# Kernel tuning notes

Hardware: AMD Instinct MI355X
Metric: run time of the kernel (lower is better)

The kernel has to match this reference:

```python
import jax, jax.numpy as jnp
jax.config.update("jax_enable_x64", True)
import numpy as np

B, S, D, H = 2, 1024, 1024, 16
DEPTH = D // H  # 64


def setup_inputs() -> dict:
    key = jax.random.key(0)
    ks = jax.random.split(key, 12)
    inp = {
        "q": jax.random.normal(ks[0], (B, S, D), jnp.float32),
        "k": jax.random.normal(ks[1], (B, S, D), jnp.float32),
        "v": jax.random.normal(ks[2], (B, S - 1, D), jnp.float32),
        "e": jnp.zeros((1,), jnp.float32),  # unused by the layer
        "mask": jax.random.randint(ks[3], (B, S - 1, S - 1), 0, 2, jnp.int32),
        "Wq": jax.random.normal(ks[4], (D, D), jnp.float32) * 0.02,
        "bq": jnp.zeros((D,), jnp.float32),
        "Wk": jax.random.normal(ks[5], (D, D), jnp.float32) * 0.02,
        "bk": jnp.zeros((D,), jnp.float32),
        "Wv": jax.random.normal(ks[6], (D, D), jnp.float32) * 0.02,
        "bv": jnp.zeros((D,), jnp.float32),
        "Wo": jax.random.normal(ks[7], (D, D), jnp.float32) * 0.02,
        "bo": jnp.zeros((D,), jnp.float32),
    }
    return inp


def _split_heads(x, b):
    # [b, s, D] -> [b, H, s, DEPTH]
    return x.reshape(b, -1, H, DEPTH).transpose(0, 2, 1, 3)


def reference(q, k, v, e, mask, Wq, bq, Wk, bk, Wv, bv, Wo, bo):
    b = q.shape[0]
    qh = _split_heads(q @ Wq + bq, b)  # [b,H,S,dh]
    kh = _split_heads(k @ Wk + bk, b)  # [b,H,S,dh]
    vh = _split_heads(v @ Wv + bv, b)  # [b,H,S-1,dh]
    # QK^T then asymmetric offset slice [1:, :-1]
    scores = jnp.einsum("bhqd,bhkd->bhqk", qh, kh)[:, :, 1:, :-1]  # [b,H,S-1,S-1]
    inv_sqrt_dk = 1.0 / jnp.sqrt(jnp.float32(DEPTH))
    nl_qk = jax.nn.relu(scores * inv_sqrt_dk).astype(jnp.float64)
    nl_qk = nl_qk + mask[:, None, :, :].astype(jnp.float64) * (-1e9)
    att_weights = jax.nn.softmax(nl_qk, axis=-1)  # fp64, [b,H,S-1,S-1]
    out = jnp.einsum("bhqk,bhkd->bhqd", att_weights, vh.astype(jnp.float64))
    out = out.transpose(0, 2, 1, 3).reshape(b, -1, H * DEPTH)  # [b,S-1,D]
    output = out.astype(jnp.float32) @ Wo + bo
    return (output, att_weights)
```

## Files before the change

kernel.cpp:

```cpp
#include <hip/hip_runtime.h>
#include <math.h>

#define HN 16
#define SEQ 1024
#define DMODEL 1024
#define DH 64
#define SM1 1023

typedef float  f32x4  __attribute__((ext_vector_type(4)));
typedef __bf16 bf16x8 __attribute__((ext_vector_type(8)));

template<int MODE>
__global__ __launch_bounds__(256)
void gemm_mfma_kernel(const float* __restrict__ X, const float* __restrict__ W,
                      const float* __restrict__ bias, float* __restrict__ out32,
                      __bf16* __restrict__ outHi, __bf16* __restrict__ outLo,
                      int M, int rows)
{
    __shared__ __align__(16) __bf16 As[2][4096];
    __shared__ __align__(16) __bf16 Bs[2][4096];

    const int t  = threadIdx.x;
    const int w  = t >> 6, l = t & 63;
    const int lr = l & 15, ls = l >> 4;
    const int m0 = blockIdx.y * 64, n0 = blockIdx.x * 64;
    const int sr  = t >> 2;
    const int skq = t & 3;
    const bool arow_ok = (m0 + sr < M);

    f32x4 acc[4];
#pragma unroll
    for (int ct = 0; ct < 4; ++ct) acc[ct] = f32x4{0.f, 0.f, 0.f, 0.f};

    const int ar   = w * 16 + lr;
    const int a_hi = ar * 128 + (((2 * ls    ) ^ (ar & 7)) << 4);
    const int a_lo = ar * 128 + (((2 * ls + 1) ^ (ar & 7)) << 4);
    const int st_hi = sr * 128 + (((2 * skq    ) ^ (sr & 7)) << 4);
    const int st_lo = sr * 128 + (((2 * skq + 1) ^ (sr & 7)) << 4);

    float4 xv0, xv1;
    float  wv[8];

    auto LOADT = [&](int k0) {
        if (arow_ok) {
            xv0 = *(const float4*)&X[(size_t)(m0 + sr) * DMODEL + k0 + skq * 8];
            xv1 = *(const float4*)&X[(size_t)(m0 + sr) * DMODEL + k0 + skq * 8 + 4];
        } else {
            xv0 = float4{0.f, 0.f, 0.f, 0.f};
            xv1 = float4{0.f, 0.f, 0.f, 0.f};
        }
#pragma unroll
        for (int e = 0; e < 8; ++e)
            wv[e] = W[(size_t)(k0 + skq * 8 + e) * DMODEL + n0 + sr];
    };
    auto WRITET = [&](int buf) {
        float xa[8] = {xv0.x, xv0.y, xv0.z, xv0.w, xv1.x, xv1.y, xv1.z, xv1.w};
        bf16x8 ah8, al8, bh8, bl8;
#pragma unroll
        for (int e = 0; e < 8; ++e) {
            __bf16 hb = (__bf16)xa[e];
            ah8[e] = hb;
            al8[e] = (__bf16)(xa[e] - (float)hb);
            __bf16 wb = (__bf16)wv[e];
            bh8[e] = wb;
            bl8[e] = (__bf16)(wv[e] - (float)wb);
        }
        *(bf16x8*)((char*)As[buf] + st_hi) = ah8;
        *(bf16x8*)((char*)As[buf] + st_lo) = al8;
        *(bf16x8*)((char*)Bs[buf] + st_hi) = bh8;
        *(bf16x8*)((char*)Bs[buf] + st_lo) = bl8;
    };

    LOADT(0);
    WRITET(0);

    for (int ks = 0; ks < 32; ++ks) {
        const int cur = ks & 1;
        if (ks < 31) LOADT((ks + 1) * 32);
        __syncthreads();

        const bf16x8 ah = *(const bf16x8*)((const char*)As[cur] + a_hi);
        const bf16x8 al = *(const bf16x8*)((const char*)As[cur] + a_lo);
#pragma unroll
        for (int ct = 0; ct < 4; ++ct) {
            const int bc   = ct * 16 + lr;
            const int b_hi = bc * 128 + (((2 * ls    ) ^ (bc & 7)) << 4);
            const int b_lo = bc * 128 + (((2 * ls + 1) ^ (bc & 7)) << 4);
            const bf16x8 bh = *(const bf16x8*)((const char*)Bs[cur] + b_hi);
            const bf16x8 bl = *(const bf16x8*)((const char*)Bs[cur] + b_lo);
            acc[ct] = __builtin_amdgcn_mfma_f32_16x16x32_bf16(ah, bh, acc[ct], 0, 0, 0);
            acc[ct] = __builtin_amdgcn_mfma_f32_16x16x32_bf16(al, bh, acc[ct], 0, 0, 0);
            acc[ct] = __builtin_amdgcn_mfma_f32_16x16x32_bf16(ah, bl, acc[ct], 0, 0, 0);
        }
        if (ks < 31) WRITET(cur ^ 1);
    }

#pragma unroll
    for (int ct = 0; ct < 4; ++ct) {
        const int n = n0 + ct * 16 + lr;
        const float bv = bias[n];
#pragma unroll
        for (int j = 0; j < 4; ++j) {
            const int m = m0 + w * 16 + ls * 4 + j;
            if (m >= M) continue;
            const float val = acc[ct][j] + bv;
            if (MODE == 1) {
                out32[(size_t)m * DMODEL + n] = val;
            } else {
                const int bb = m / rows, s = m - bb * rows;
                const __bf16 hb = (__bf16)val;
                const __bf16 lb = (__bf16)(val - (float)hb);
                size_t idx;
                if (MODE == 0)
                    idx = (((size_t)(bb * HN + (n >> 6)) * SEQ + s) << 6) + (n & 63);
                else
                    idx = (((size_t)(bb * HN + (n >> 6)) * DH + (n & 63)) << 10) + s;
                outHi[idx] = hb; outLo[idx] = lb;
            }
        }
    }
}

__global__ __launch_bounds__(256)
void mask_pack_kernel(const int* __restrict__ mask, unsigned int* __restrict__ mb)
{
    const int row = blockIdx.x * 4 + (threadIdx.x >> 6);
    const int l   = threadIdx.x & 63;
    if (row >= 2 * SM1) return;
    const int* mrow = mask + (size_t)row * SM1;
    unsigned int* out = mb + (size_t)row * 32;
#pragma unroll
    for (int i = 0; i < 16; ++i) {
        const int c = i * 64 + l;
        const bool mv = (c < SM1) && (mrow[c] != 0);
        unsigned long long bal = __ballot(mv);
        if (l == 0) {
            out[i * 2]     = (unsigned int)bal;
            out[i * 2 + 1] = (unsigned int)(bal >> 32);
        }
    }
}

__global__ __launch_bounds__(512, 4)
void attn_fused_kernel(const __bf16* __restrict__ qhi, const __bf16* __restrict__ qlo,
                       const __bf16* __restrict__ khi, const __bf16* __restrict__ klo,
                       const __bf16* __restrict__ vthi, const __bf16* __restrict__ vtlo,
                       const unsigned int* __restrict__ mbG,
                       float* __restrict__ att, float* __restrict__ ctx)
{
    __shared__ __align__(16) char QE[64 * 528];
    __shared__ __align__(16) char KV[32768];
    __shared__ unsigned int mbitsT[32][64];
    __shared__ float invs[64];
    __shared__ float partial[64][2];

    const int id  = blockIdx.x;
    const int xcd = id & 7, slot = id >> 3;
    const int bh  = xcd + 8 * (slot >> 4);
    const int b   = bh >> 4, h = bh & 15;
    const int q0  = (slot & 15) * 64;

    const int t = threadIdx.x, w = t >> 6, l = t & 63;
    const int lr = l & 15, ls = l >> 4;
    const int g = w & 3, p = w >> 2;

    int k_roff[4], k_doff[4], k_soff[4];
#pragma unroll
    for (int it = 0; it < 4; ++it) {
        const int idk = t + it * 512;
        const int r = idk >> 4, cw = idk & 15;
        k_roff[it] = r;
        k_soff[it] = (cw & 7) * 8 + ((cw >> 3) ? 1 : 0) * 0;
        k_doff[it] = r * 256 + ((cw ^ (r & 15)) << 4);
    }
    int k_plane[4];
#pragma unroll
    for (int it = 0; it < 4; ++it) {
        const int idk = t + it * 512;
        k_plane[it] = (idk & 15) >> 3;
    }
    int v_droff[4], v_soff[4], v_doff[4], v_plane[4];
#pragma unroll
    for (int it = 0; it < 4; ++it) {
        const int idv = t + it * 512;
        const int dr = idv >> 5, cw = idv & 31;
        v_droff[it] = dr;
        v_plane[it] = cw >> 4;
        v_soff[it]  = (cw & 15) * 8;
        v_doff[it]  = dr * 512 + ((cw ^ (dr & 31)) << 4);
    }

    bf16x8 kr[4], vr[4];

#pragma unroll
    for (int it = 0; it < 2; ++it) {
        const int idq = t + it * 512;
        const int r = idq >> 4, cw = idq & 15;
        const int plane = cw >> 3, s = cw & 7;
        int qrow = q0 + r + 1; if (qrow > 1023) qrow = 1023;
        const __bf16* src = plane ? qlo : qhi;
        bf16x8 vv = *(const bf16x8*)&src[((size_t)bh * SEQ + qrow) * DH + s * 8];
        *(bf16x8*)(QE + r * 256 + ((cw ^ (r & 15)) << 4)) = vv;
    }
#pragma unroll
    for (int it = 0; it < 4; ++it) {
        const int idm = t + it * 512;
        const int cw = idm & 31, r = idm >> 5;
        const int rr = q0 + r;
        mbitsT[cw][r] = (rr < SM1) ? mbG[((size_t)b * SM1 + rr) * 32 + cw] : 0u;
    }
    __syncthreads();

    const int ar = g * 16 + lr;
    const bf16x8 a0h = *(const bf16x8*)(QE + ar * 256 + (((ls     ) ^ lr) << 4));
    const bf16x8 a1h = *(const bf16x8*)(QE + ar * 256 + ((( 4 + ls) ^ lr) << 4));
    const bf16x8 a0l = *(const bf16x8*)(QE + ar * 256 + ((( 8 + ls) ^ lr) << 4));
    const bf16x8 a1l = *(const bf16x8*)(QE + ar * 256 + (((12 + ls) ^ lr) << 4));
    __syncthreads();

#define LOADK(c0_)                                                              \
    {                                                                           \
        _Pragma("unroll")                                                       \
        for (int it = 0; it < 4; ++it) {                                        \
            int krow = (c0_) + k_roff[it]; if (krow > 1023) krow = 1023;        \
            const __bf16* src = k_plane[it] ? klo : khi;                        \
            kr[it] = *(const bf16x8*)&src[((size_t)bh * SEQ + krow) * DH + k_soff[it]]; \
        }                                                                       \
    }
#define WRITEK()                                                                \
    {                                                                           \
        _Pragma("unroll")                                                       \
        for (int it = 0; it < 4; ++it)                                          \
            *(bf16x8*)(KV + k_doff[it]) = kr[it];                               \
    }
#define LOADV(c0_)                                                              \
    {                                                                           \
        _Pragma("unroll")                                                       \
        for (int it = 0; it < 4; ++it) {                                        \
            const __bf16* src = v_plane[it] ? vtlo : vthi;                      \
            vr[it] = *(const bf16x8*)&src[(((size_t)bh * DH + v_droff[it]) << 10) + (c0_) + v_soff[it]]; \
        }                                                                       \
    }
#define WRITEV()                                                                \
    {                                                                           \
        _Pragma("unroll")                                                       \
        for (int it = 0; it < 4; ++it)                                          \
            *(bf16x8*)(KV + v_doff[it]) = vr[it];                               \
    }

    float rsum[4] = {0.f, 0.f, 0.f, 0.f};
    LOADK(0);
    WRITEK();
    for (int kt = 0; kt < 8; ++kt) {
        const int c0 = kt * 128;
        if (kt < 7) LOADK(c0 + 128);
        __syncthreads();

#pragma unroll
        for (int i = 0; i < 4; ++i) {
            const int ct = p * 4 + i;
            const int kr16 = ct * 16 + lr;
            const bf16x8 b0h = *(const bf16x8*)(KV + kr16 * 256 + (((ls     ) ^ lr) << 4));
            const bf16x8 b1h = *(const bf16x8*)(KV + kr16 * 256 + ((( 4 + ls) ^ lr) << 4));
            const bf16x8 b0l = *(const bf16x8*)(KV + kr16 * 256 + ((( 8 + ls) ^ lr) << 4));
            const bf16x8 b1l = *(const bf16x8*)(KV + kr16 * 256 + (((12 + ls) ^ lr) << 4));

            f32x4 acc = {0.f, 0.f, 0.f, 0.f};
            __builtin_amdgcn_s_setprio(1);
            acc = __builtin_amdgcn_mfma_f32_16x16x32_bf16(a0h, b0h, acc, 0, 0, 0);
            acc = __builtin_amdgcn_mfma_f32_16x16x32_bf16(a0l, b0h, acc, 0, 0, 0);
            acc = __builtin_amdgcn_mfma_f32_16x16x32_bf16(a0h, b0l, acc, 0, 0, 0);
            acc = __builtin_amdgcn_mfma_f32_16x16x32_bf16(a1h, b1h, acc, 0, 0, 0);
            acc = __builtin_amdgcn_mfma_f32_16x16x32_bf16(a1l, b1h, acc, 0, 0, 0);
            acc = __builtin_amdgcn_mfma_f32_16x16x32_bf16(a1h, b1l, acc, 0, 0, 0);
            __builtin_amdgcn_s_setprio(0);

            const int c = c0 + ct * 16 + lr;
            const int wmi = kt * 4 + (ct >> 1);
#pragma unroll
            for (int j = 0; j < 4; ++j) {
                const int r = q0 + g * 16 + ls * 4 + j;
                if (r < SM1 && c < SM1) {
                    float sc = fmaxf(acc[j] * 0.125f, 0.f);
                    const unsigned int wm = mbitsT[wmi][g * 16 + ls * 4 + j];
                    if ((wm >> ((ct & 1) * 16 + lr)) & 1u) sc = -1e9f;
                    rsum[j] += __expf(sc);
                }
            }
        }
        __syncthreads();
        if (kt < 7) WRITEK();
    }

    LOADK(0);

#pragma unroll
    for (int j = 0; j < 4; ++j) {
        rsum[j] += __shfl_xor(rsum[j], 1, 64);
        rsum[j] += __shfl_xor(rsum[j], 2, 64);
        rsum[j] += __shfl_xor(rsum[j], 4, 64);
        rsum[j] += __shfl_xor(rsum[j], 8, 64);
    }
    if (lr == 0) {
#pragma unroll
        for (int j = 0; j < 4; ++j)
            partial[g * 16 + ls * 4 + j][p] = rsum[j];
    }
    __syncthreads();
    if (t < 64) {
        const float s = partial[t][0] + partial[t][1];
        invs[t] = (q0 + t < SM1) ? 1.0f / s : 0.f;
    }
    __syncthreads();
    float inv4[4];
#pragma unroll
    for (int j = 0; j < 4; ++j) inv4[j] = invs[g * 16 + ls * 4 + j];

    float* E = (float*)QE;
    f32x4 oacc[4];
#pragma unroll
    for (int ct = 0; ct < 4; ++ct) oacc[ct] = f32x4{0.f, 0.f, 0.f, 0.f};

    for (int kt = 0; kt < 8; ++kt) {
        const int c0 = kt * 128;
        __syncthreads();
        WRITEK();
        LOADV(c0);
        __syncthreads();

#pragma unroll
        for (int i = 0; i < 4; ++i) {
            const int ct = p * 4 + i;
            const int kr16 = ct * 16 + lr;
            const bf16x8 b0h = *(const bf16x8*)(KV + kr16 * 256 + (((ls     ) ^ lr) << 4));
            const bf16x8 b1h = *(const bf16x8*)(KV + kr16 * 256 + ((( 4 + ls) ^ lr) << 4));
            const bf16x8 b0l = *(const bf16x8*)(KV + kr16 * 256 + ((( 8 + ls) ^ lr) << 4));
            const bf16x8 b1l = *(const bf16x8*)(KV + kr16 * 256 + (((12 + ls) ^ lr) << 4));

            f32x4 acc = {0.f, 0.f, 0.f, 0.f};
            __builtin_amdgcn_s_setprio(1);
            acc = __builtin_amdgcn_mfma_f32_16x16x32_bf16(a0h, b0h, acc, 0, 0, 0);
            acc = __builtin_amdgcn_mfma_f32_16x16x32_bf16(a0l, b0h, acc, 0, 0, 0);
            acc = __builtin_amdgcn_mfma_f32_16x16x32_bf16(a0h, b0l, acc, 0, 0, 0);
            acc = __builtin_amdgcn_mfma_f32_16x16x32_bf16(a1h, b1h, acc, 0, 0, 0);
            acc = __builtin_amdgcn_mfma_f32_16x16x32_bf16(a1l, b1h, acc, 0, 0, 0);
            acc = __builtin_amdgcn_mfma_f32_16x16x32_bf16(a1h, b1l, acc, 0, 0, 0);
            __builtin_amdgcn_s_setprio(0);

            const int c = c0 + ct * 16 + lr;
            const int wmi = kt * 4 + (ct >> 1);
#pragma unroll
            for (int j = 0; j < 4; ++j) {
                const int r = q0 + g * 16 + ls * 4 + j;
                float v = 0.f;
                if (r < SM1 && c < SM1) {
                    float sc = fmaxf(acc[j] * 0.125f, 0.f);
                    const unsigned int wm = mbitsT[wmi][g * 16 + ls * 4 + j];
                    if ((wm >> ((ct & 1) * 16 + lr)) & 1u) sc = -1e9f;
                    v = __expf(sc) * inv4[j];
                }
                E[(g * 16 + ls * 4 + j) * 132 + ct * 16 + lr] = v;
            }
        }
        if (kt < 7) LOADK(c0 + 128);
        __syncthreads();

        WRITEV();
#pragma unroll
        for (int it = 0; it < 4; ++it) {
            const int idw = t + it * 512;
            const int r = idw >> 5, q4 = idw & 31;
            const int rr = q0 + r, cc = c0 + q4 * 4;
            if (rr < SM1) {
                f32x4 vv = *(const f32x4*)&E[r * 132 + q4 * 4];
                float* dst = &att[((size_t)bh * SM1 + rr) * SM1 + cc];
                if (cc + 4 <= SM1) {
                    __builtin_nontemporal_store(vv, (f32x4*)dst);
                } else {
                    if (cc + 0 < SM1) dst[0] = vv.x;
                    if (cc + 1 < SM1) dst[1] = vv.y;
                    if (cc + 2 < SM1) dst[2] = vv.z;
                }
            }
        }
        __syncthreads();

#pragma unroll
        for (int m = 0; m < 2; ++m) {
            const int ks = p * 2 + m;
            const int pr = g * 16 + lr;
            const f32x4 p0 = *(const f32x4*)&E[pr * 132 + ks * 32 + ls * 8];
            const f32x4 p1 = *(const f32x4*)&E[pr * 132 + ks * 32 + ls * 8 + 4];
            float pf[8] = {p0.x, p0.y, p0.z, p0.w, p1.x, p1.y, p1.z, p1.w};
            bf16x8 ph, pl;
#pragma unroll
            for (int e = 0; e < 8; ++e) {
                const __bf16 hb = (__bf16)pf[e];
                ph[e] = hb;
                pl[e] = (__bf16)(pf[e] - (float)hb);
            }
#pragma unroll
            for (int ct = 0; ct < 4; ++ct) {
                const int vr16 = ct * 16 + lr;
                const int hslot = ((ks * 4 + ls) ^ (vr16 & 31));
                const int lslot = ((16 + ks * 4 + ls) ^ (vr16 & 31));
                const bf16x8 vh = *(const bf16x8*)(KV + vr16 * 512 + (hslot << 4));
                const bf16x8 vl = *(const bf16x8*)(KV + vr16 * 512 + (lslot << 4));
                __builtin_amdgcn_s_setprio(1);
                oacc[ct] = __builtin_amdgcn_mfma_f32_16x16x32_bf16(ph, vh, oacc[ct], 0, 0, 0);
                oacc[ct] = __builtin_amdgcn_mfma_f32_16x16x32_bf16(pl, vh, oacc[ct], 0, 0, 0);
                oacc[ct] = __builtin_amdgcn_mfma_f32_16x16x32_bf16(ph, vl, oacc[ct], 0, 0, 0);
                __builtin_amdgcn_s_setprio(0);
            }
        }
    }

    __syncthreads();
    float* red = (float*)QE;
    if (p == 1) {
#pragma unroll
        for (int ct = 0; ct < 4; ++ct)
#pragma unroll
            for (int j = 0; j < 4; ++j)
                red[(g * 16 + ls * 4 + j) * 68 + ct * 16 + lr] = oacc[ct][j];
    }
    __syncthreads();
    if (p == 0) {
#pragma unroll
        for (int ct = 0; ct < 4; ++ct)
#pragma unroll
            for (int j = 0; j < 4; ++j) {
                const int r = q0 + g * 16 + ls * 4 + j;
                if (r < SM1)
                    ctx[((size_t)b * SM1 + r) * DMODEL + h * DH + ct * 16 + lr] =
                        oacc[ct][j] + red[(g * 16 + ls * 4 + j) * 68 + ct * 16 + lr];
            }
    }
#undef LOADK
#undef WRITEK
#undef LOADV
#undef WRITEV
}

extern "C" void kernel_launch(void* const* d_in, const int* in_sizes, int n_in,
                              void* d_out, int out_size, void* d_ws, size_t ws_size,
                              hipStream_t stream) {
    const float* q    = (const float*)d_in[0];
    const float* k    = (const float*)d_in[1];
    const float* v    = (const float*)d_in[2];
    const int*   mask = (const int*)  d_in[4];
    const float* Wq   = (const float*)d_in[5];
    const float* bq   = (const float*)d_in[6];
    const float* Wk   = (const float*)d_in[7];
    const float* bk   = (const float*)d_in[8];
    const float* Wv   = (const float*)d_in[9];
    const float* bv   = (const float*)d_in[10];
    const float* Wo   = (const float*)d_in[11];
    const float* bo   = (const float*)d_in[12];

    float* out0 = (float*)d_out;
    float* att  = out0 + (size_t)2 * SM1 * DMODEL;

    const size_t NQ  = (size_t)2 * HN * SEQ * DH;
    const size_t NVT = (size_t)2 * HN * DH * 1024;
    __bf16* ws16 = (__bf16*)d_ws;
    __bf16* qhi  = ws16;
    __bf16* qlo  = qhi + NQ;
    __bf16* khi  = qlo + NQ;
    __bf16* klo  = khi + NQ;
    __bf16* vthi = klo + NQ;
    __bf16* vtlo = vthi + NVT;
    float*  ctx  = (float*)(vtlo + NVT);
    unsigned int* mbG = (unsigned int*)(ctx + (size_t)2 * SM1 * DMODEL);

    (void)hipMemsetAsync(vthi, 0, 2 * NVT * sizeof(__bf16), stream);

    mask_pack_kernel<<<dim3(512), 256, 0, stream>>>(mask, mbG);

    gemm_mfma_kernel<0><<<dim3(16, 32), 256, 0, stream>>>(q, Wq, bq, nullptr, qhi, qlo, 2 * SEQ, SEQ);
    gemm_mfma_kernel<0><<<dim3(16, 32), 256, 0, stream>>>(k, Wk, bk, nullptr, khi, klo, 2 * SEQ, SEQ);
    gemm_mfma_kernel<2><<<dim3(16, 32), 256, 0, stream>>>(v, Wv, bv, nullptr, vthi, vtlo, 2 * SM1, SM1);

    attn_fused_kernel<<<dim3(512), 512, 0, stream>>>(qhi, qlo, khi, klo, vthi, vtlo, mbG, att, ctx);

    gemm_mfma_kernel<1><<<dim3(16, 32), 256, 0, stream>>>(ctx, Wo, bo, out0, nullptr, nullptr, 2 * SM1, SM1);
}
```

Measured before the change: 276.3 us.

## Stream K/V tiles into LDS via direct global-to-LDS loads with double-buffered K

Replaces register-staged K, V and Q loads, which went global to registers and then to LDS, with 16-byte global_load_lds transfers. The XOR swizzle moves from the LDS destination to the global source address. The attention loops switch from 128-column to 64-column tiles, with a double-buffered K tile and a separate V tile, and the second pass drops one barrier per iteration. The aim is to free registers and hide load latency behind the MFMA work. The cost is twice as many tile iterations and barriers, and correctness depends on the asynchronous LDS writes being complete before each barrier.

New measurement: 244.6 us. -11.5%, faster.

```diff
diff --git a/kernel.cpp b/kernel.cpp
--- a/kernel.cpp
+++ b/kernel.cpp
@@ -9,6 +9,10 @@
 
 typedef float  f32x4  __attribute__((ext_vector_type(4)));
 typedef __bf16 bf16x8 __attribute__((ext_vector_type(8)));
+
+#define GLD16(gsrc, ldst) \
+    __builtin_amdgcn_global_load_lds((const __attribute__((address_space(1))) void*)(gsrc), \
+                                     (__attribute__((address_space(3))) void*)(ldst), 16, 0, 0)
 
 template<int MODE>
 __global__ __launch_bounds__(256)
@@ -148,8 +152,9 @@
                        const unsigned int* __restrict__ mbG,
                        float* __restrict__ att, float* __restrict__ ctx)
 {
-    __shared__ __align__(16) char QE[64 * 528];
-    __shared__ __align__(16) char KV[32768];
+    __shared__ __align__(16) char QE[17408];
+    __shared__ __align__(16) char Kb[2][16384];
+    __shared__ __align__(16) char Vb[16384];
     __shared__ unsigned int mbitsT[32][64];
     __shared__ float invs[64];
     __shared__ float partial[64][2];
@@ -164,44 +169,39 @@
     const int lr = l & 15, ls = l >> 4;
     const int g = w & 3, p = w >> 2;
 
-    int k_roff[4], k_doff[4], k_soff[4];
-#pragma unroll
-    for (int it = 0; it < 4; ++it) {
-        const int idk = t + it * 512;
-        const int r = idk >> 4, cw = idk & 15;
-        k_roff[it] = r;
-        k_soff[it] = (cw & 7) * 8 + ((cw >> 3) ? 1 : 0) * 0;
-        k_doff[it] = r * 256 + ((cw ^ (r & 15)) << 4);
-    }
-    int k_plane[4];
-#pragma unroll
-    for (int it = 0; it < 4; ++it) {
-        const int idk = t + it * 512;
-        k_plane[it] = (idk & 15) >> 3;
-    }
-    int v_droff[4], v_soff[4], v_doff[4], v_plane[4];
-#pragma unroll
-    for (int it = 0; it < 4; ++it) {
-        const int idv = t + it * 512;
-        const int dr = idv >> 5, cw = idv & 31;
-        v_droff[it] = dr;
-        v_plane[it] = cw >> 4;
-        v_soff[it]  = (cw & 15) * 8;
-        v_doff[it]  = dr * 512 + ((cw ^ (dr & 31)) << 4);
-    }
-
-    bf16x8 kr[4], vr[4];
-
-#pragma unroll
-    for (int it = 0; it < 2; ++it) {
-        const int idq = t + it * 512;
-        const int r = idq >> 4, cw = idq & 15;
-        const int plane = cw >> 3, s = cw & 7;
+#define KDMA(c0_, b_) {                                                         \
+    _Pragma("unroll")                                                           \
+    for (int i_ = 0; i_ < 2; ++i_) {                                            \
+        const int seg_ = w * 2 + i_;                                            \
+        const int r_ = seg_ * 4 + (l >> 4);                                     \
+        const int cw_ = (l & 15) ^ (r_ & 15);                                   \
+        int krow_ = (c0_) + r_; if (krow_ > 1023) krow_ = 1023;                 \
+        const __bf16* src_ = ((cw_ >> 3) ? klo : khi)                           \
+            + ((size_t)bh * SEQ + krow_) * DH + (cw_ & 7) * 8;                  \
+        GLD16(src_, Kb[b_] + seg_ * 1024);                                      \
+    } }
+#define VDMA(c0_) {                                                             \
+    _Pragma("unroll")                                                           \
+    for (int i_ = 0; i_ < 2; ++i_) {                                            \
+        const int seg_ = w * 2 + i_;                                            \
+        const int dr_ = seg_ * 4 + (l >> 4);                                    \
+        const int cw_ = (l & 15) ^ (dr_ & 15);                                  \
+        const __bf16* src_ = ((cw_ >> 3) ? vtlo : vthi)                         \
+            + (((size_t)bh * DH + dr_) << 10) + (c0_) + (cw_ & 7) * 8;          \
+        GLD16(src_, Vb + seg_ * 1024);                                          \
+    } }
+
+#pragma unroll
+    for (int i = 0; i < 2; ++i) {
+        const int seg = w * 2 + i;
+        const int r = seg * 4 + (l >> 4);
+        const int cw = (l & 15) ^ (r & 15);
         int qrow = q0 + r + 1; if (qrow > 1023) qrow = 1023;
-        const __bf16* src = plane ? qlo : qhi;
-        bf16x8 vv = *(const bf16x8*)&src[((size_t)bh * SEQ + qrow) * DH + s * 8];
-        *(bf16x8*)(QE + r * 256 + ((cw ^ (r & 15)) << 4)) = vv;
-    }
+        const __bf16* src = ((cw >> 3) ? qlo : qhi)
+            + ((size_t)bh * SEQ + qrow) * DH + (cw & 7) * 8;
+        GLD16(src, QE + seg * 1024);
+    }
+    KDMA(0, 0);
 #pragma unroll
     for (int it = 0; it < 4; ++it) {
         const int idm = t + it * 512;
@@ -211,59 +211,27 @@
     }
     __syncthreads();
 
-    const int ar = g * 16 + lr;
-    const bf16x8 a0h = *(const bf16x8*)(QE + ar * 256 + (((ls     ) ^ lr) << 4));
-    const bf16x8 a1h = *(const bf16x8*)(QE + ar * 256 + ((( 4 + ls) ^ lr) << 4));
-    const bf16x8 a0l = *(const bf16x8*)(QE + ar * 256 + ((( 8 + ls) ^ lr) << 4));
-    const bf16x8 a1l = *(const bf16x8*)(QE + ar * 256 + (((12 + ls) ^ lr) << 4));
+    const int arow = g * 16 + lr;
+    const bf16x8 a0h = *(const bf16x8*)(QE + arow * 256 + (((ls     ) ^ lr) << 4));
+    const bf16x8 a1h = *(const bf16x8*)(QE + arow * 256 + ((( 4 + ls) ^ lr) << 4));
+    const bf16x8 a0l = *(const bf16x8*)(QE + arow * 256 + ((( 8 + ls) ^ lr) << 4));
+    const bf16x8 a1l = *(const bf16x8*)(QE + arow * 256 + (((12 + ls) ^ lr) << 4));
     __syncthreads();
 
-#define LOADK(c0_)                                                              \
-    {                                                                           \
-        _Pragma("unroll")                                                       \
-        for (int it = 0; it < 4; ++it) {                                        \
-            int krow = (c0_) + k_roff[it]; if (krow > 1023) krow = 1023;        \
-            const __bf16* src = k_plane[it] ? klo : khi;                        \
-            kr[it] = *(const bf16x8*)&src[((size_t)bh * SEQ + krow) * DH + k_soff[it]]; \
-        }                                                                       \
-    }
-#define WRITEK()                                                                \
-    {                                                                           \
-        _Pragma("unroll")                                                       \
-        for (int it = 0; it < 4; ++it)                                          \
-            *(bf16x8*)(KV + k_doff[it]) = kr[it];                               \
-    }
-#define LOADV(c0_)                                                              \
-    {                                                                           \
-        _Pragma("unroll")                                                       \
-        for (int it = 0; it < 4; ++it) {                                        \
-            const __bf16* src = v_plane[it] ? vtlo : vthi;                      \
-            vr[it] = *(const bf16x8*)&src[(((size_t)bh * DH + v_droff[it]) << 10) + (c0_) + v_soff[it]]; \
-        }                                                                       \
-    }
-#define WRITEV()                                                                \
-    {                                                                           \
-        _Pragma("unroll")                                                       \
-        for (int it = 0; it < 4; ++it)                                          \
-            *(bf16x8*)(KV + v_doff[it]) = vr[it];                               \
-    }
-
     float rsum[4] = {0.f, 0.f, 0.f, 0.f};
-    LOADK(0);
-    WRITEK();
-    for (int kt = 0; kt < 8; ++kt) {
-        const int c0 = kt * 128;
-        if (kt < 7) LOADK(c0 + 128);
-        __syncthreads();
-
-#pragma unroll
-        for (int i = 0; i < 4; ++i) {
-            const int ct = p * 4 + i;
+    for (int kt = 0; kt < 16; ++kt) {
+        const int c0 = kt * 64;
+        const char* KB = Kb[kt & 1];
+        if (kt < 15) KDMA(c0 + 64, (kt + 1) & 1);
+
+#pragma unroll
+        for (int i = 0; i < 2; ++i) {
+            const int ct = p * 2 + i;
             const int kr16 = ct * 16 + lr;
-            const bf16x8 b0h = *(const bf16x8*)(KV + kr16 * 256 + (((ls     ) ^ lr) << 4));
-            const bf16x8 b1h = *(const bf16x8*)(KV + kr16 * 256 + ((( 4 + ls) ^ lr) << 4));
-            const bf16x8 b0l = *(const bf16x8*)(KV + kr16 * 256 + ((( 8 + ls) ^ lr) << 4));
-            const bf16x8 b1l = *(const bf16x8*)(KV + kr16 * 256 + (((12 + ls) ^ lr) << 4));
+            const bf16x8 b0h = *(const bf16x8*)(KB + kr16 * 256 + (((ls     ) ^ lr) << 4));
+            const bf16x8 b1h = *(const bf16x8*)(KB + kr16 * 256 + ((( 4 + ls) ^ lr) << 4));
+            const bf16x8 b0l = *(const bf16x8*)(KB + kr16 * 256 + ((( 8 + ls) ^ lr) << 4));
+            const bf16x8 b1l = *(const bf16x8*)(KB + kr16 * 256 + (((12 + ls) ^ lr) << 4));
 
             f32x4 acc = {0.f, 0.f, 0.f, 0.f};
             __builtin_amdgcn_s_setprio(1);
@@ -276,7 +244,7 @@
             __builtin_amdgcn_s_setprio(0);
 
             const int c = c0 + ct * 16 + lr;
-            const int wmi = kt * 4 + (ct >> 1);
+            const int wmi = kt * 2 + (ct >> 1);
 #pragma unroll
             for (int j = 0; j < 4; ++j) {
                 const int r = q0 + g * 16 + ls * 4 + j;
@@ -289,10 +257,9 @@
             }
         }
         __syncthreads();
-        if (kt < 7) WRITEK();
-    }
-
-    LOADK(0);
+    }
+
+    KDMA(0, 0);
 
 #pragma unroll
     for (int j = 0; j < 4; ++j) {
@@ -321,21 +288,20 @@
 #pragma unroll
     for (int ct = 0; ct < 4; ++ct) oacc[ct] = f32x4{0.f, 0.f, 0.f, 0.f};
 
-    for (int kt = 0; kt < 8; ++kt) {
-        const int c0 = kt * 128;
-        __syncthreads();
-        WRITEK();
-        LOADV(c0);
-        __syncthreads();
-
-#pragma unroll
-        for (int i = 0; i < 4; ++i) {
-            const int ct = p * 4 + i;
+    for (int kt = 0; kt < 16; ++kt) {
+        const int c0 = kt * 64;
+        const char* KB = Kb[kt & 1];
+        VDMA(c0);
+        if (kt < 15) KDMA(c0 + 64, (kt + 1) & 1);
+
+#pragma unroll
+        for (int i = 0; i < 2; ++i) {
+            const int ct = p * 2 + i;
             const int kr16 = ct * 16 + lr;
-            const bf16x8 b0h = *(const bf16x8*)(KV + kr16 * 256 + (((ls     ) ^ lr) << 4));
-            const bf16x8 b1h = *(const bf16x8*)(KV + kr16 * 256 + ((( 4 + ls) ^ lr) << 4));
-            const bf16x8 b0l = *(const bf16x8*)(KV + kr16 * 256 + ((( 8 + ls) ^ lr) << 4));
-            const bf16x8 b1l = *(const bf16x8*)(KV + kr16 * 256 + (((12 + ls) ^ lr) << 4));
+            const bf16x8 b0h = *(const bf16x8*)(KB + kr16 * 256 + (((ls     ) ^ lr) << 4));
+            const bf16x8 b1h = *(const bf16x8*)(KB + kr16 * 256 + ((( 4 + ls) ^ lr) << 4));
+            const bf16x8 b0l = *(const bf16x8*)(KB + kr16 * 256 + ((( 8 + ls) ^ lr) << 4));
+            const bf16x8 b1l = *(const bf16x8*)(KB + kr16 * 256 + (((12 + ls) ^ lr) << 4));
 
             f32x4 acc = {0.f, 0.f, 0.f, 0.f};
             __builtin_amdgcn_s_setprio(1);
@@ -348,7 +314,7 @@
             __builtin_amdgcn_s_setprio(0);
 
             const int c = c0 + ct * 16 + lr;
-            const int wmi = kt * 4 + (ct >> 1);
+            const int wmi = kt * 2 + (ct >> 1);
 #pragma unroll
             for (int j = 0; j < 4; ++j) {
                 const int r = q0 + g * 16 + ls * 4 + j;
@@ -359,20 +325,18 @@
                     if ((wm >> ((ct & 1) * 16 + lr)) & 1u) sc = -1e9f;
                     v = __expf(sc) * inv4[j];
                 }
-                E[(g * 16 + ls * 4 + j) * 132 + ct * 16 + lr] = v;
-            }
-        }
-        if (kt < 7) LOADK(c0 + 128);
+                E[(g * 16 + ls * 4 + j) * 68 + ct * 16 + lr] = v;
+            }
+        }
         __syncthreads();
 
-        WRITEV();
-#pragma unroll
-        for (int it = 0; it < 4; ++it) {
+#pragma unroll
+        for (int it = 0; it < 2; ++it) {
             const int idw = t + it * 512;
-            const int r = idw >> 5, q4 = idw & 31;
+            const int r = idw >> 4, q4 = idw & 15;
             const int rr = q0 + r, cc = c0 + q4 * 4;
             if (rr < SM1) {
-                f32x4 vv = *(const f32x4*)&E[r * 132 + q4 * 4];
+                f32x4 vv = *(const f32x4*)&E[r * 68 + q4 * 4];
                 float* dst = &att[((size_t)bh * SM1 + rr) * SM1 + cc];
                 if (cc + 4 <= SM1) {
                     __builtin_nontemporal_store(vv, (f32x4*)dst);
@@ -383,14 +347,11 @@
                 }
             }
         }
-        __syncthreads();
-
-#pragma unroll
-        for (int m = 0; m < 2; ++m) {
-            const int ks = p * 2 + m;
+
+        {
             const int pr = g * 16 + lr;
-            const f32x4 p0 = *(const f32x4*)&E[pr * 132 + ks * 32 + ls * 8];
-            const f32x4 p1 = *(const f32x4*)&E[pr * 132 + ks * 32 + ls * 8 + 4];
+            const f32x4 p0 = *(const f32x4*)&E[pr * 68 + p * 32 + ls * 8];
+            const f32x4 p1 = *(const f32x4*)&E[pr * 68 + p * 32 + ls * 8 + 4];
             float pf[8] = {p0.x, p0.y, p0.z, p0.w, p1.x, p1.y, p1.z, p1.w};
             bf16x8 ph, pl;
 #pragma unroll
@@ -402,10 +363,8 @@
 #pragma unroll
             for (int ct = 0; ct < 4; ++ct) {
                 const int vr16 = ct * 16 + lr;
-                const int hslot = ((ks * 4 + ls) ^ (vr16 & 31));
-                const int lslot = ((16 + ks * 4 + ls) ^ (vr16 & 31));
-                const bf16x8 vh = *(const bf16x8*)(KV + vr16 * 512 + (hslot << 4));
-                const bf16x8 vl = *(const bf16x8*)(KV + vr16 * 512 + (lslot << 4));
+                const bf16x8 vh = *(const bf16x8*)(Vb + vr16 * 256 + (((p * 4 + ls    ) ^ lr) << 4));
+                const bf16x8 vl = *(const bf16x8*)(Vb + vr16 * 256 + (((8 + p * 4 + ls) ^ lr) << 4));
                 __builtin_amdgcn_s_setprio(1);
                 oacc[ct] = __builtin_amdgcn_mfma_f32_16x16x32_bf16(ph, vh, oacc[ct], 0, 0, 0);
                 oacc[ct] = __builtin_amdgcn_mfma_f32_16x16x32_bf16(pl, vh, oacc[ct], 0, 0, 0);
@@ -413,9 +372,9 @@
                 __builtin_amdgcn_s_setprio(0);
             }
         }
-    }
-
-    __syncthreads();
+        __syncthreads();
+    }
+
     float* red = (float*)QE;
     if (p == 1) {
 #pragma unroll
@@ -436,10 +395,8 @@
                         oacc[ct][j] + red[(g * 16 + ls * 4 + j) * 68 + ct * 16 + lr];
             }
     }
-#undef LOADK
-#undef WRITEK
-#undef LOADV
-#undef WRITEV
+#undef KDMA
+#undef VDMA
 }
 
 extern "C" void kernel_launch(void* const* d_in, const int* in_sizes, int n_in,
```
